# Optimization experiments

Hardware: AMD Instinct MI355X
Metric: run time of the kernel (lower is better)

## Reference

```python
import jax, jax.numpy as jnp
import numpy as np

N = 20000      # nodes
E = 200000     # edges (before self loops)
H = 8          # heads
C = 256        # out_channels per head
IN = 256       # in_channels
OUT = 250      # final linear out


def setup_inputs() -> dict:
    key = jax.random.key(0)
    ks = jax.random.split(key, 8)
    x = jax.random.normal(ks[0], (N, IN), jnp.float32)
    edge_index = jax.random.randint(ks[1], (2, E), 0, N)
    # GATConv params (lin has no bias in PyG; bias is on the conv output)
    W_gat = jax.random.normal(ks[2], (IN, H * C), jnp.float32) * 0.02
    att_src = jax.random.normal(ks[3], (H, C), jnp.float32) * 0.1
    att_dst = jax.random.normal(ks[4], (H, C), jnp.float32) * 0.1
    b_gat = jnp.zeros((H * C,), jnp.float32)
    # conv1: 1x1 conv with 1 in/out channel -> scalar weight + scalar bias
    conv_w = jax.random.normal(ks[5], (), jnp.float32)
    conv_b = jnp.zeros((), jnp.float32)
    W_lin = jax.random.normal(ks[6], (C, OUT), jnp.float32) * 0.02
    b_lin = jnp.zeros((OUT,), jnp.float32)
    return dict(x=x, edge_index=edge_index, W_gat=W_gat, att_src=att_src,
                att_dst=att_dst, b_gat=b_gat, conv_w=conv_w, conv_b=conv_b,
                W_lin=W_lin, b_lin=b_lin)


def reference(x, edge_index, W_gat, att_src, att_dst, b_gat, conv_w, conv_b, W_lin, b_lin):
    # --- GATConv (PyG defaults: add_self_loops=True, negative_slope=0.2, concat=True) ---
    loops = jnp.arange(N)
    src = jnp.concatenate([edge_index[0], loops])  # [E+N]
    dst = jnp.concatenate([edge_index[1], loops])
    xh = (x @ W_gat).reshape(N, H, C)              # [N,H,C]
    a_s = jnp.einsum('nhc,hc->nh', xh, att_src)    # [N,H]
    a_d = jnp.einsum('nhc,hc->nh', xh, att_dst)
    e = jax.nn.leaky_relu(a_s[src] + a_d[dst], 0.2)  # [E+N, H]
    # segment softmax over edges sharing a destination node
    m = jax.ops.segment_max(e, dst, num_segments=N)
    m = jnp.where(jnp.isfinite(m), m, 0.0)
    ex = jnp.exp(e - m[dst])
    s = jax.ops.segment_sum(ex, dst, num_segments=N)
    alpha = ex / (s[dst] + 1e-16)                  # [E+N, H]
    msg = xh[src] * alpha[:, :, None]              # [E+N, H, C]  (dominant traffic)
    agg = jax.ops.segment_sum(msg, dst, num_segments=N)  # [N,H,C]
    agg = agg + b_gat.reshape(H, C)
    # --- head split / pool / 1x1 conv / head softmax / fuse ---
    z = agg.transpose(1, 0, 2)                     # [H,N,C]  (torch z is [H,1,N,C])
    pooled = z.mean(axis=(1, 2))                   # [H] global avg pool
    g = jax.nn.relu(pooled * conv_w + conv_b)
    w = jax.nn.softmax(g, axis=0)                  # softmax over heads (dim=0)
    fuse = jnp.einsum('hnc,h->nc', z, w)           # sum over heads of z * w
    Hf = jax.nn.relu(fuse + x)                     # residual with input features
    return Hf @ W_lin + b_lin                      # [N, 250]
```

## Files before the change

### kernel.cpp

```cpp
#include <hip/hip_runtime.h>
#include <hip/hip_bf16.h>


typedef __attribute__((ext_vector_type(8))) short short8v;
typedef __attribute__((ext_vector_type(4))) float float4v;

__device__ __forceinline__ unsigned f2bfu(float f) {
  unsigned u = __float_as_uint(f);
  return (u + 0x7fffu + ((u >> 16) & 1u)) >> 16;
}
__device__ __forceinline__ float bfu_lo(unsigned u) { return __uint_as_float(u << 16); }
__device__ __forceinline__ float bfu_hi(unsigned u) { return __uint_as_float(u & 0xffff0000u); }
__device__ __forceinline__ unsigned pack2(float a, float b) { return f2bfu(a) | (f2bfu(b) << 16); }

__device__ __forceinline__ void ld8(const float* p, float* v) {
  float4 a = ((const float4*)p)[0], b = ((const float4*)p)[1];
  v[0] = a.x; v[1] = a.y; v[2] = a.z; v[3] = a.w;
  v[4] = b.x; v[5] = b.y; v[6] = b.z; v[7] = b.w;
}

__device__ __forceinline__ float bcast(float x, int e) {
  return __uint_as_float((unsigned)__builtin_amdgcn_readlane((int)__float_as_uint(x), e));
}

__device__ __forceinline__ void gll16(const void* g, void* l) {
  __builtin_amdgcn_global_load_lds(
      (__attribute__((address_space(1))) void*)const_cast<void*>(g),
      (__attribute__((address_space(3))) void*)(l), 16, 0, 0);
}

__global__ __launch_bounds__(256) void prep1_kernel(
    const float* __restrict__ W_lin, short* __restrict__ wlT,
    const float* __restrict__ W, const float* __restrict__ att_s,
    const float* __restrict__ att_d, float* __restrict__ ws_s,
    float* __restrict__ ws_d, float* __restrict__ ws_r,
    const int* __restrict__ ei, int* __restrict__ deg) {
  __shared__ float smem[4096];
  int b = blockIdx.x;
  int t = threadIdx.x;
  if (b < 64) {
    float (*tile)[33] = (float(*)[33])smem;
    int tx = t & 31, ty = t >> 5;
    int c0 = (b & 7) * 32, r0 = (b >> 3) * 32;
    #pragma unroll
    for (int j = ty; j < 32; j += 8) {
      int r = r0 + j, c = c0 + tx;
      tile[j][tx] = (c < 250) ? W_lin[(size_t)r * 250 + c] : 0.f;
    }
    __syncthreads();
    #pragma unroll
    for (int j = ty; j < 32; j += 8) {
      int c = c0 + j, r = r0 + tx;
      wlT[(size_t)c * 256 + r] = (short)f2bfu(tile[tx][j]);
    }
  } else if (b < 96) {
    float* sas = smem;
    float* sad = smem + 2048;
    for (int i = t; i < 2048; i += 256) { sas[i] = att_s[i]; sad[i] = att_d[i]; }
    __syncthreads();
    int kk = t >> 5, h = (t >> 2) & 7, q = t & 3;
    int k = (b - 64) * 8 + kk;
    const float4* wr = (const float4*)(W + (size_t)k * 2048 + h * 256 + q * 64);
    const float* as = sas + h * 256 + q * 64;
    const float* ad = sad + h * 256 + q * 64;
    float s = 0.f, dd = 0.f, r = 0.f;
    #pragma unroll
    for (int c4 = 0; c4 < 16; ++c4) {
      float4 wv = wr[c4];
      int c = c4 * 4;
      s  += wv.x * as[c] + wv.y * as[c + 1] + wv.z * as[c + 2] + wv.w * as[c + 3];
      dd += wv.x * ad[c] + wv.y * ad[c + 1] + wv.z * ad[c + 2] + wv.w * ad[c + 3];
      r  += wv.x + wv.y + wv.z + wv.w;
    }
    #pragma unroll
    for (int off = 1; off < 4; off <<= 1) {
      s += __shfl_xor(s, off);
      dd += __shfl_xor(dd, off);
      r += __shfl_xor(r, off);
    }
    if (q == 0) {
      int g = k * 8 + h;
      ws_s[g] = s;
      ws_d[g] = dd;
      ws_r[g] = r;
    }
  } else {
    int e = (b - 96) * 256 + t;
    if (e < 200000) atomicAdd(&deg[ei[200000 + e]], 1);
  }
}

__global__ __launch_bounds__(256) void asd_kernel(const float* __restrict__ x,
    const float* __restrict__ ws_s, const float* __restrict__ ws_d,
    const float* __restrict__ ws_r, float* __restrict__ a_s,
    float* __restrict__ a_d, float* __restrict__ rs, short* __restrict__ x_bf) {
  __shared__ float ls[2048], ld2[2048], lr[2048];
  int tid = threadIdx.x;
  for (int i = tid; i < 2048; i += 256) { ls[i] = ws_s[i]; ld2[i] = ws_d[i]; lr[i] = ws_r[i]; }
  __syncthreads();
  int node = blockIdx.x * 32 + (tid >> 3);
  int h = tid & 7;
  const float4* xr = (const float4*)(x + (size_t)node * 256);
  float as = 0.f, ad = 0.f, rr = 0.f;
  #pragma unroll 1
  for (int g = 0; g < 8; ++g) {
    bool own = (g == h);
    int bufi[16];
    #pragma unroll
    for (int j = 0; j < 8; ++j) {
      int k4 = g * 8 + j;
      float4 v = xr[k4];
      int k8 = k4 * 32 + h;
      as += v.x * ls[k8] + v.y * ls[k8 + 8] + v.z * ls[k8 + 16] + v.w * ls[k8 + 24];
      ad += v.x * ld2[k8] + v.y * ld2[k8 + 8] + v.z * ld2[k8 + 16] + v.w * ld2[k8 + 24];
      rr += v.x * lr[k8] + v.y * lr[k8 + 8] + v.z * lr[k8 + 16] + v.w * lr[k8 + 24];
      bufi[2 * j] = (int)pack2(v.x, v.y);
      bufi[2 * j + 1] = (int)pack2(v.z, v.w);
    }
    if (own) {
      int4* dst = (int4*)(x_bf + (size_t)node * 256 + h * 32);
      dst[0] = make_int4(bufi[0], bufi[1], bufi[2], bufi[3]);
      dst[1] = make_int4(bufi[4], bufi[5], bufi[6], bufi[7]);
      dst[2] = make_int4(bufi[8], bufi[9], bufi[10], bufi[11]);
      dst[3] = make_int4(bufi[12], bufi[13], bufi[14], bufi[15]);
    }
  }
  a_s[node * 8 + h] = as;
  a_d[node * 8 + h] = ad;
  rs[node * 8 + h] = rr;
}

__global__ __launch_bounds__(256, 2) void gemm_fused_kernel(
    const short* __restrict__ u, const short* __restrict__ wmixT,
    const short* __restrict__ wlT, short* __restrict__ Hf,
    float* __restrict__ out, const float* __restrict__ fb,
    const float* __restrict__ x, const float* __restrict__ b_lin, int M) {
  __shared__ short lA[64 * 128];
  __shared__ short lB[256 * 128];
  int tid = threadIdx.x;
  int wave = tid >> 6, lane = tid & 63;
  int m0 = blockIdx.x << 6;
  int lr = lane & 15, lq = lane >> 4;
  int lrow4 = lane >> 4;
  int pch = lane & 15;

  float4v acc[4][4];
  #pragma unroll
  for (int i = 0; i < 4; ++i)
    #pragma unroll
    for (int j = 0; j < 4; ++j) acc[i][j] = (float4v){0.f, 0.f, 0.f, 0.f};

  int rowlA[4], growA[4], logA[4];
  #pragma unroll
  for (int it = 0; it < 4; ++it) {
    rowlA[it] = wave * 16 + it * 4 + lrow4;
    int grow = m0 + rowlA[it];
    if (grow >= M) grow = M - 1;
    growA[it] = grow;
    logA[it] = pch ^ (rowlA[it] & 7);
  }
  int rowB[16], logB[16];
  #pragma unroll
  for (int it = 0; it < 16; ++it) {
    rowB[it] = wave * 64 + it * 4 + lrow4;
    logB[it] = pch ^ (rowB[it] & 7);
  }

  for (int t = 0; t < 16; ++t) {
    int k0 = t << 7;
    __syncthreads();
    #pragma unroll
    for (int it = 0; it < 4; ++it)
      gll16(u + (size_t)growA[it] * 2048 + logA[it] * 8 + k0, lA + (wave * 16 + it * 4) * 128);
    #pragma unroll
    for (int it = 0; it < 16; ++it)
      gll16(wmixT + (size_t)rowB[it] * 2048 + logB[it] * 8 + k0, lB + (wave * 64 + it * 4) * 128);
    __syncthreads();
    #pragma unroll
    for (int ks = 0; ks < 4; ++ks) {
      int phys = ((ks * 4 + lq) ^ (lr & 7)) * 8;
      short8v af[4], bfv[4];
      #pragma unroll
      for (int i = 0; i < 4; ++i)
        af[i] = *(const short8v*)(lA + (i * 16 + lr) * 128 + phys);
      #pragma unroll
      for (int j = 0; j < 4; ++j)
        bfv[j] = *(const short8v*)(lB + (wave * 64 + j * 16 + lr) * 128 + phys);
      #pragma unroll
      for (int i = 0; i < 4; ++i)
        #pragma unroll
        for (int j = 0; j < 4; ++j)
          acc[i][j] = __builtin_amdgcn_mfma_f32_16x16x32_bf16(af[i], bfv[j], acc[i][j], 0, 0, 0);
    }
  }
  #pragma unroll
  for (int i = 0; i < 4; ++i) {
    #pragma unroll
    for (int jj = 0; jj < 4; ++jj) {
      int row = m0 + i * 16 + lq * 4 + jj;
      if (row >= M) continue;
      #pragma unroll
      for (int j = 0; j < 4; ++j) {
        int col = wave * 64 + j * 16 + lr;
        float o = acc[i][j][jj] + fb[col] + x[(size_t)row * 256 + col];
        Hf[(size_t)row * 256 + col] = (short)f2bfu(fmaxf(o, 0.f));
      }
    }
  }

  #pragma unroll
  for (int i = 0; i < 4; ++i)
    #pragma unroll
    for (int j = 0; j < 4; ++j) acc[i][j] = (float4v){0.f, 0.f, 0.f, 0.f};

  for (int t = 0; t < 2; ++t) {
    int k0 = t << 7;
    __syncthreads();
    #pragma unroll
    for (int it = 0; it < 4; ++it)
      gll16(Hf + (size_t)growA[it] * 256 + logA[it] * 8 + k0, lA + (wave * 16 + it * 4) * 128);
    #pragma unroll
    for (int it = 0; it < 16; ++it)
      gll16(wlT + (size_t)rowB[it] * 256 + logB[it] * 8 + k0, lB + (wave * 64 + it * 4) * 128);
    __syncthreads();
    #pragma unroll
    for (int ks = 0; ks < 4; ++ks) {
      int phys = ((ks * 4 + lq) ^ (lr & 7)) * 8;
      short8v af[4], bfv[4];
      #pragma unroll
      for (int i = 0; i < 4; ++i)
        af[i] = *(const short8v*)(lA + (i * 16 + lr) * 128 + phys);
      #pragma unroll
      for (int j = 0; j < 4; ++j)
        bfv[j] = *(const short8v*)(lB + (wave * 64 + j * 16 + lr) * 128 + phys);
      #pragma unroll
      for (int i = 0; i < 4; ++i)
        #pragma unroll
        for (int j = 0; j < 4; ++j)
          acc[i][j] = __builtin_amdgcn_mfma_f32_16x16x32_bf16(af[i], bfv[j], acc[i][j], 0, 0, 0);
    }
  }
  #pragma unroll
  for (int i = 0; i < 4; ++i) {
    #pragma unroll
    for (int jj = 0; jj < 4; ++jj) {
      int row = m0 + i * 16 + lq * 4 + jj;
      if (row >= M) continue;
      #pragma unroll
      for (int j = 0; j < 4; ++j) {
        int col = wave * 64 + j * 16 + lr;
        if (col < 250) out[(size_t)row * 250 + col] = acc[i][j][jj] + b_lin[col];
      }
    }
  }
}


__global__ __launch_bounds__(1024) void scan_kernel(const int* __restrict__ deg,
                                                    int* __restrict__ rowptr,
                                                    int* __restrict__ cursor, int n) {
  __shared__ int part[1024];
  int t = threadIdx.x;
  int base = t * 20;
  int loc[20];
  int run = 0;
  #pragma unroll
  for (int j = 0; j < 20; ++j) {
    int idx = base + j;
    int v = (idx < n) ? deg[idx] : 0;
    loc[j] = run;
    run += v;
  }
  part[t] = run;
  __syncthreads();
  for (int off = 1; off < 1024; off <<= 1) {
    int add = (t >= off) ? part[t - off] : 0;
    __syncthreads();
    part[t] += add;
    __syncthreads();
  }
  int off0 = (t > 0) ? part[t - 1] : 0;
  #pragma unroll
  for (int j = 0; j < 20; ++j) {
    int idx = base + j;
    if (idx < n) {
      int v = off0 + loc[j];
      rowptr[idx] = v;
      cursor[idx] = v;
    }
  }
  if (t == 1023) rowptr[n] = part[1023];
}

__global__ void scatter_kernel(const int* __restrict__ ei, int* __restrict__ cursor,
                               int* __restrict__ csr_src, int E) {
  int e = blockIdx.x * 256 + threadIdx.x;
  if (e < E) {
    int pos = atomicAdd(&cursor[ei[E + e]], 1);
    csr_src[pos] = ei[e];
  }
}

__global__ __launch_bounds__(256) void alphaz_kernel(
    const short* __restrict__ x_bf, const float* __restrict__ a_s,
    const float* __restrict__ a_d, const float* __restrict__ rs,
    const int* __restrict__ rowptr, const int* __restrict__ csr,
    short* __restrict__ u, float* __restrict__ pp) {
  int d = blockIdx.x * 4 + (threadIdx.x >> 6);
  int lane = threadIdx.x & 63;
  int half = lane >> 5;
  int cl = (lane & 31) * 8;
  int beg = rowptr[d];
  int deg = rowptr[d + 1] - beg;
  int nb = deg + 1;

  float ad8[8];
  ld8(a_d + (size_t)d * 8, ad8);

  float acc[8][8];
  #pragma unroll
  for (int h = 0; h < 8; ++h)
    #pragma unroll
    for (int c = 0; c < 8; ++c) acc[h][c] = 0.f;
  float s8[8] = {0, 0, 0, 0, 0, 0, 0, 0};
  float p8[8] = {0, 0, 0, 0, 0, 0, 0, 0};

  for (int base = 0; base < nb; base += 64) {
    int i = base + lane;
    bool act = i < nb;
    int srcv = d;
    if (i < deg) srcv = csr[beg + i];
    float ex[8];
    {
      float t8[8], r8[8];
      ld8(a_s + (size_t)srcv * 8, t8);
      ld8(rs + (size_t)srcv * 8, r8);
      #pragma unroll
      for (int h = 0; h < 8; ++h) {
        float e = t8[h] + ad8[h];
        e = (e > 0.f) ? e : 0.2f * e;
        float xx = act ? __expf(e) : 0.f;
        ex[h] = xx;
        s8[h] += xx;
        p8[h] += xx * r8[h];
      }
    }
    int cnt = nb - base;
    if (cnt > 64) cnt = 64;
    int e = 0;
    for (; e + 1 < cnt; e += 2) {
      int s0 = __builtin_amdgcn_readlane(srcv, e);
      int s1 = __builtin_amdgcn_readlane(srcv, e + 1);
      int ss = half ? s1 : s0;
      uint4 v = *(const uint4*)(x_bf + (size_t)ss * 256 + cl);
      float q[8];
      #pragma unroll
      for (int h = 0; h < 8; ++h) {
        float qa = bcast(ex[h], e), qb = bcast(ex[h], e + 1);
        q[h] = half ? qb : qa;
      }
      float xv[8];
      xv[0] = bfu_lo(v.x); xv[1] = bfu_hi(v.x);
      xv[2] = bfu_lo(v.y); xv[3] = bfu_hi(v.y);
      xv[4] = bfu_lo(v.z); xv[5] = bfu_hi(v.z);
      xv[6] = bfu_lo(v.w); xv[7] = bfu_hi(v.w);
      #pragma unroll
      for (int h = 0; h < 8; ++h)
        #pragma unroll
        for (int c = 0; c < 8; ++c) acc[h][c] += q[h] * xv[c];
    }
    if (e < cnt) {
      int s0 = __builtin_amdgcn_readlane(srcv, e);
      uint4 v = *(const uint4*)(x_bf + (size_t)s0 * 256 + cl);
      float q[8];
      #pragma unroll
      for (int h = 0; h < 8; ++h) q[h] = half ? 0.f : bcast(ex[h], e);
      float xv[8];
      xv[0] = bfu_lo(v.x); xv[1] = bfu_hi(v.x);
      xv[2] = bfu_lo(v.y); xv[3] = bfu_hi(v.y);
      xv[4] = bfu_lo(v.z); xv[5] = bfu_hi(v.z);
      xv[6] = bfu_lo(v.w); xv[7] = bfu_hi(v.w);
      #pragma unroll
      for (int h = 0; h < 8; ++h)
        #pragma unroll
        for (int c = 0; c < 8; ++c) acc[h][c] += q[h] * xv[c];
    }
  }

  #pragma unroll
  for (int h = 0; h < 8; ++h)
    #pragma unroll
    for (int c = 0; c < 8; ++c) acc[h][c] += __shfl_xor(acc[h][c], 32);
  #pragma unroll
  for (int off = 1; off < 64; off <<= 1)
    #pragma unroll
    for (int h = 0; h < 8; ++h) {
      s8[h] += __shfl_xor(s8[h], off);
      p8[h] += __shfl_xor(p8[h], off);
    }
  float inv[8];
  #pragma unroll
  for (int h = 0; h < 8; ++h) inv[h] = 1.f / (s8[h] + 1e-16f);

  if (half == 0) {
    #pragma unroll
    for (int h = 0; h < 8; ++h) {
      uint4 ov;
      ov.x = pack2(acc[h][0] * inv[h], acc[h][1] * inv[h]);
      ov.y = pack2(acc[h][2] * inv[h], acc[h][3] * inv[h]);
      ov.z = pack2(acc[h][4] * inv[h], acc[h][5] * inv[h]);
      ov.w = pack2(acc[h][6] * inv[h], acc[h][7] * inv[h]);
      *(uint4*)(u + (size_t)d * 2048 + h * 256 + cl) = ov;
    }
  }
  if (lane == 0) {
    float pn[8];
    #pragma unroll
    for (int h = 0; h < 8; ++h) pn[h] = p8[h] * inv[h];
    ((float4*)(pp + (size_t)d * 8))[0] = make_float4(pn[0], pn[1], pn[2], pn[3]);
    ((float4*)(pp + (size_t)d * 8))[1] = make_float4(pn[4], pn[5], pn[6], pn[7]);
  }
}

__global__ __launch_bounds__(256) void reduce_pp_kernel(const float* __restrict__ pp,
                                                        float* __restrict__ pooled) {
  int tid = threadIdx.x;
  float loc[8] = {0, 0, 0, 0, 0, 0, 0, 0};
  for (int r = blockIdx.x * 256 + tid; r < 20000; r += 80 * 256) {
    float t[8];
    ld8(pp + (size_t)r * 8, t);
    #pragma unroll
    for (int h = 0; h < 8; ++h) loc[h] += t[h];
  }
  #pragma unroll
  for (int off = 1; off < 64; off <<= 1)
    #pragma unroll
    for (int h = 0; h < 8; ++h) loc[h] += __shfl_xor(loc[h], off);
  __shared__ float sred[4][8];
  int wave = tid >> 6, lane = tid & 63;
  if (lane == 0) {
    #pragma unroll
    for (int h = 0; h < 8; ++h) sred[wave][h] = loc[h];
  }
  __syncthreads();
  if (tid < 8) {
    atomicAdd(&pooled[tid], sred[0][tid] + sred[1][tid] + sred[2][tid] + sred[3][tid]);
  }
}

__global__ __launch_bounds__(256) void headwfb_kernel(const float* __restrict__ pooled,
    const float* __restrict__ b_gat, const float* __restrict__ conv_w,
    const float* __restrict__ conv_b, float* __restrict__ wsoft,
    float* __restrict__ fb) {
  __shared__ float sb[8];
  __shared__ float sw[8];
  int t = threadIdx.x;
  float v = 0.f;
  #pragma unroll
  for (int j = 0; j < 8; ++j) v += b_gat[t * 8 + j];
  #pragma unroll
  for (int off = 1; off < 32; off <<= 1) v += __shfl_xor(v, off);
  if ((t & 31) == 0) sb[t >> 5] = v;
  __syncthreads();
  if (t == 0) {
    const float invNC = 1.0f / (20000.0f * 256.0f);
    float g[8];
    float mx = -1e30f;
    #pragma unroll
    for (int h = 0; h < 8; ++h) {
      float pm = (pooled[h] + 20000.0f * sb[h]) * invNC;
      float gv = pm * conv_w[0] + conv_b[0];
      gv = fmaxf(gv, 0.f);
      g[h] = gv;
      mx = fmaxf(mx, gv);
    }
    float ssum = 0.f;
    #pragma unroll
    for (int h = 0; h < 8; ++h) { g[h] = __expf(g[h] - mx); ssum += g[h]; }
    #pragma unroll
    for (int h = 0; h < 8; ++h) {
      float w = g[h] / ssum;
      wsoft[h] = w;
      sw[h] = w;
    }
  }
  __syncthreads();
  float a = 0.f;
  #pragma unroll
  for (int h = 0; h < 8; ++h) a += sw[h] * b_gat[h * 256 + t];
  fb[t] = a;
}

__global__ void wmix_kernel(const float* __restrict__ W, const float* __restrict__ wsoft,
                            short* __restrict__ out) {
  __shared__ float tile[32][33];
  int tx = threadIdx.x, ty = threadIdx.y;
  int h = blockIdx.z;
  float wh = wsoft[h];
  int c0 = blockIdx.x * 32, k0 = blockIdx.y * 32;
  #pragma unroll
  for (int j = ty; j < 32; j += 8)
    tile[j][tx] = W[(size_t)(k0 + j) * 2048 + h * 256 + c0 + tx];
  __syncthreads();
  #pragma unroll
  for (int j = ty; j < 32; j += 8)
    out[(size_t)(c0 + j) * 2048 + h * 256 + k0 + tx] = (short)f2bfu(wh * tile[tx][j]);
}

extern "C" void kernel_launch(void* const* d_in, const int* in_sizes, int n_in,
                              void* d_out, int out_size, void* d_ws, size_t ws_size,
                              hipStream_t stream) {
  (void)in_sizes; (void)n_in; (void)out_size; (void)ws_size;
  const float* x      = (const float*)d_in[0];
  const int*   ei     = (const int*)d_in[1];
  const float* W_gat  = (const float*)d_in[2];
  const float* att_s  = (const float*)d_in[3];
  const float* att_d  = (const float*)d_in[4];
  const float* b_gat  = (const float*)d_in[5];
  const float* conv_w = (const float*)d_in[6];
  const float* conv_b = (const float*)d_in[7];
  const float* W_lin  = (const float*)d_in[8];
  const float* b_lin  = (const float*)d_in[9];
  float* out = (float*)d_out;

  char* p = (char*)d_ws;
  size_t off = 0;
  auto alloc = [&](size_t bytes) -> void* {
    void* r = p + off;
    off = (off + bytes + 255) & ~(size_t)255;
    return r;
  };
  short* x_bf   = (short*)alloc((size_t)20000 * 256 * 2);
  short* wmixT  = (short*)alloc((size_t)256 * 2048 * 2);
  short* wlT    = (short*)alloc((size_t)256 * 256 * 2);
  float* ws_s   = (float*)alloc(2048 * 4);
  float* ws_d   = (float*)alloc(2048 * 4);
  float* ws_r   = (float*)alloc(2048 * 4);
  float* a_s    = (float*)alloc((size_t)20000 * 8 * 4);
  float* a_d    = (float*)alloc((size_t)20000 * 8 * 4);
  float* rs     = (float*)alloc((size_t)20000 * 8 * 4);
  int*   deg    = (int*)alloc(20000 * 4);
  float* pooled = (float*)alloc(8 * 4);
  float* wsoft  = (float*)alloc(8 * 4);
  float* fb     = (float*)alloc(256 * 4);
  int*   rowptr = (int*)alloc(20001 * 4);
  int*   cursor = (int*)alloc(20000 * 4);
  int*   csr    = (int*)alloc(200000 * 4);
  float* pp     = (float*)alloc((size_t)20000 * 8 * 4);
  short* u      = (short*)alloc((size_t)20000 * 2048 * 2);
  short* Hf     = x_bf;

  hipMemsetAsync(deg, 0, 20000 * 4, stream);
  hipMemsetAsync(pooled, 0, 8 * 4, stream);

  prep1_kernel<<<878, 256, 0, stream>>>(W_lin, wlT, W_gat, att_s, att_d,
                                        ws_s, ws_d, ws_r, ei, deg);
  scan_kernel<<<1, 1024, 0, stream>>>(deg, rowptr, cursor, 20000);
  asd_kernel<<<625, 256, 0, stream>>>(x, ws_s, ws_d, ws_r, a_s, a_d, rs, x_bf);
  scatter_kernel<<<782, 256, 0, stream>>>(ei, cursor, csr, 200000);
  alphaz_kernel<<<5000, 256, 0, stream>>>(x_bf, a_s, a_d, rs, rowptr, csr, u, pp);
  reduce_pp_kernel<<<80, 256, 0, stream>>>(pp, pooled);
  headwfb_kernel<<<1, 256, 0, stream>>>(pooled, b_gat, conv_w, conv_b, wsoft, fb);
  wmix_kernel<<<dim3(8, 8, 8), dim3(32, 8), 0, stream>>>(W_gat, wsoft, wmixT);
  gemm_fused_kernel<<<313, 256, 0, stream>>>(u, wmixT, wlT, Hf, out, fb, x, b_lin, 20000);
}
```

Measured before the change: 208.2 us.

## Compute pooled projection from aggregated features instead of per-node rs term

Drops the per-node rs dot product from the asd kernel and its gather in alphaz. The pooled contribution is now computed after aggregation by dotting the normalized aggregate against ws_r with a wave reduction. Alphaz is also restructured so each lane owns 4 channels and processes one edge per iteration, replacing the two-edges-per-iteration half-wave split and its final cross-half shuffle. This lowers register pressure and removes one memory stream, but issues narrower loads and adds a per-node reduction.

After: 194.4 us. -6.6%, faster.

```diff
diff --git a/kernel.cpp b/kernel.cpp
--- a/kernel.cpp
+++ b/kernel.cpp
@@ -92,16 +92,15 @@
 
 __global__ __launch_bounds__(256) void asd_kernel(const float* __restrict__ x,
     const float* __restrict__ ws_s, const float* __restrict__ ws_d,
-    const float* __restrict__ ws_r, float* __restrict__ a_s,
-    float* __restrict__ a_d, float* __restrict__ rs, short* __restrict__ x_bf) {
-  __shared__ float ls[2048], ld2[2048], lr[2048];
+    float* __restrict__ a_s, float* __restrict__ a_d, short* __restrict__ x_bf) {
+  __shared__ float ls[2048], ld2[2048];
   int tid = threadIdx.x;
-  for (int i = tid; i < 2048; i += 256) { ls[i] = ws_s[i]; ld2[i] = ws_d[i]; lr[i] = ws_r[i]; }
+  for (int i = tid; i < 2048; i += 256) { ls[i] = ws_s[i]; ld2[i] = ws_d[i]; }
   __syncthreads();
   int node = blockIdx.x * 32 + (tid >> 3);
   int h = tid & 7;
   const float4* xr = (const float4*)(x + (size_t)node * 256);
-  float as = 0.f, ad = 0.f, rr = 0.f;
+  float as = 0.f, ad = 0.f;
   #pragma unroll 1
   for (int g = 0; g < 8; ++g) {
     bool own = (g == h);
@@ -113,7 +112,6 @@
       int k8 = k4 * 32 + h;
       as += v.x * ls[k8] + v.y * ls[k8 + 8] + v.z * ls[k8 + 16] + v.w * ls[k8 + 24];
       ad += v.x * ld2[k8] + v.y * ld2[k8 + 8] + v.z * ld2[k8 + 16] + v.w * ld2[k8 + 24];
-      rr += v.x * lr[k8] + v.y * lr[k8 + 8] + v.z * lr[k8 + 16] + v.w * lr[k8 + 24];
       bufi[2 * j] = (int)pack2(v.x, v.y);
       bufi[2 * j + 1] = (int)pack2(v.z, v.w);
     }
@@ -127,7 +125,6 @@
   }
   a_s[node * 8 + h] = as;
   a_d[node * 8 + h] = ad;
-  rs[node * 8 + h] = rr;
 }
 
 __global__ __launch_bounds__(256, 2) void gemm_fused_kernel(
@@ -303,13 +300,12 @@
 
 __global__ __launch_bounds__(256) void alphaz_kernel(
     const short* __restrict__ x_bf, const float* __restrict__ a_s,
-    const float* __restrict__ a_d, const float* __restrict__ rs,
+    const float* __restrict__ a_d, const float* __restrict__ ws_r,
     const int* __restrict__ rowptr, const int* __restrict__ csr,
     short* __restrict__ u, float* __restrict__ pp) {
   int d = blockIdx.x * 4 + (threadIdx.x >> 6);
   int lane = threadIdx.x & 63;
-  int half = lane >> 5;
-  int cl = (lane & 31) * 8;
+  int cl = lane * 4;
   int beg = rowptr[d];
   int deg = rowptr[d + 1] - beg;
   int nb = deg + 1;
@@ -317,13 +313,12 @@
   float ad8[8];
   ld8(a_d + (size_t)d * 8, ad8);
 
-  float acc[8][8];
+  float acc[8][4];
   #pragma unroll
   for (int h = 0; h < 8; ++h)
     #pragma unroll
-    for (int c = 0; c < 8; ++c) acc[h][c] = 0.f;
+    for (int c = 0; c < 4; ++c) acc[h][c] = 0.f;
   float s8[8] = {0, 0, 0, 0, 0, 0, 0, 0};
-  float p8[8] = {0, 0, 0, 0, 0, 0, 0, 0};
 
   for (int base = 0; base < nb; base += 64) {
     int i = base + lane;
@@ -332,9 +327,8 @@
     if (i < deg) srcv = csr[beg + i];
     float ex[8];
     {
-      float t8[8], r8[8];
+      float t8[8];
       ld8(a_s + (size_t)srcv * 8, t8);
-      ld8(rs + (size_t)srcv * 8, r8);
       #pragma unroll
       for (int h = 0; h < 8; ++h) {
         float e = t8[h] + ad8[h];
@@ -342,83 +336,66 @@
         float xx = act ? __expf(e) : 0.f;
         ex[h] = xx;
         s8[h] += xx;
-        p8[h] += xx * r8[h];
       }
     }
     int cnt = nb - base;
     if (cnt > 64) cnt = 64;
-    int e = 0;
-    for (; e + 1 < cnt; e += 2) {
-      int s0 = __builtin_amdgcn_readlane(srcv, e);
-      int s1 = __builtin_amdgcn_readlane(srcv, e + 1);
-      int ss = half ? s1 : s0;
-      uint4 v = *(const uint4*)(x_bf + (size_t)ss * 256 + cl);
+    for (int e = 0; e < cnt; ++e) {
+      int sb = __builtin_amdgcn_readlane(srcv, e);
+      uint2 v = *(const uint2*)(x_bf + (size_t)sb * 256 + cl);
       float q[8];
       #pragma unroll
+      for (int h = 0; h < 8; ++h) q[h] = bcast(ex[h], e);
+      float xv0 = bfu_lo(v.x), xv1 = bfu_hi(v.x);
+      float xv2 = bfu_lo(v.y), xv3 = bfu_hi(v.y);
+      #pragma unroll
       for (int h = 0; h < 8; ++h) {
-        float qa = bcast(ex[h], e), qb = bcast(ex[h], e + 1);
-        q[h] = half ? qb : qa;
+        acc[h][0] += q[h] * xv0;
+        acc[h][1] += q[h] * xv1;
+        acc[h][2] += q[h] * xv2;
+        acc[h][3] += q[h] * xv3;
       }
-      float xv[8];
-      xv[0] = bfu_lo(v.x); xv[1] = bfu_hi(v.x);
-      xv[2] = bfu_lo(v.y); xv[3] = bfu_hi(v.y);
-      xv[4] = bfu_lo(v.z); xv[5] = bfu_hi(v.z);
-      xv[6] = bfu_lo(v.w); xv[7] = bfu_hi(v.w);
-      #pragma unroll
-      for (int h = 0; h < 8; ++h)
-        #pragma unroll
-        for (int c = 0; c < 8; ++c) acc[h][c] += q[h] * xv[c];
-    }
-    if (e < cnt) {
-      int s0 = __builtin_amdgcn_readlane(srcv, e);
-      uint4 v = *(const uint4*)(x_bf + (size_t)s0 * 256 + cl);
-      float q[8];
-      #pragma unroll
-      for (int h = 0; h < 8; ++h) q[h] = half ? 0.f : bcast(ex[h], e);
-      float xv[8];
-      xv[0] = bfu_lo(v.x); xv[1] = bfu_hi(v.x);
-      xv[2] = bfu_lo(v.y); xv[3] = bfu_hi(v.y);
-      xv[4] = bfu_lo(v.z); xv[5] = bfu_hi(v.z);
-      xv[6] = bfu_lo(v.w); xv[7] = bfu_hi(v.w);
-      #pragma unroll
-      for (int h = 0; h < 8; ++h)
-        #pragma unroll
-        for (int c = 0; c < 8; ++c) acc[h][c] += q[h] * xv[c];
-    }
-  }
-
-  #pragma unroll
-  for (int h = 0; h < 8; ++h)
-    #pragma unroll
-    for (int c = 0; c < 8; ++c) acc[h][c] += __shfl_xor(acc[h][c], 32);
+    }
+  }
+
   #pragma unroll
   for (int off = 1; off < 64; off <<= 1)
     #pragma unroll
-    for (int h = 0; h < 8; ++h) {
-      s8[h] += __shfl_xor(s8[h], off);
-      p8[h] += __shfl_xor(p8[h], off);
-    }
+    for (int h = 0; h < 8; ++h) s8[h] += __shfl_xor(s8[h], off);
   float inv[8];
   #pragma unroll
   for (int h = 0; h < 8; ++h) inv[h] = 1.f / (s8[h] + 1e-16f);
 
-  if (half == 0) {
-    #pragma unroll
-    for (int h = 0; h < 8; ++h) {
-      uint4 ov;
-      ov.x = pack2(acc[h][0] * inv[h], acc[h][1] * inv[h]);
-      ov.y = pack2(acc[h][2] * inv[h], acc[h][3] * inv[h]);
-      ov.z = pack2(acc[h][4] * inv[h], acc[h][5] * inv[h]);
-      ov.w = pack2(acc[h][6] * inv[h], acc[h][7] * inv[h]);
-      *(uint4*)(u + (size_t)d * 2048 + h * 256 + cl) = ov;
-    }
-  }
+  #pragma unroll
+  for (int h = 0; h < 8; ++h) {
+    uint2 ov;
+    ov.x = pack2(acc[h][0] * inv[h], acc[h][1] * inv[h]);
+    ov.y = pack2(acc[h][2] * inv[h], acc[h][3] * inv[h]);
+    *(uint2*)(u + (size_t)d * 2048 + h * 256 + cl) = ov;
+  }
+
+  float ppl[8] = {0, 0, 0, 0, 0, 0, 0, 0};
+  {
+    const float4* wr = (const float4*)(ws_r + (size_t)cl * 8);
+    #pragma unroll
+    for (int c = 0; c < 4; ++c) {
+      float4 wa = wr[c * 2], wb = wr[c * 2 + 1];
+      float zc[8];
+      #pragma unroll
+      for (int h = 0; h < 8; ++h) zc[h] = acc[h][c] * inv[h];
+      ppl[0] += zc[0] * wa.x; ppl[1] += zc[1] * wa.y;
+      ppl[2] += zc[2] * wa.z; ppl[3] += zc[3] * wa.w;
+      ppl[4] += zc[4] * wb.x; ppl[5] += zc[5] * wb.y;
+      ppl[6] += zc[6] * wb.z; ppl[7] += zc[7] * wb.w;
+    }
+  }
+  #pragma unroll
+  for (int off = 1; off < 64; off <<= 1)
+    #pragma unroll
+    for (int h = 0; h < 8; ++h) ppl[h] += __shfl_xor(ppl[h], off);
   if (lane == 0) {
-    float pn[8];
-    #pragma unroll
-    for (int h = 0; h < 8; ++h) pn[h] = p8[h] * inv[h];
-    ((float4*)(pp + (size_t)d * 8))[0] = make_float4(pn[0], pn[1], pn[2], pn[3]);
-    ((float4*)(pp + (size_t)d * 8))[1] = make_float4(pn[4], pn[5], pn[6], pn[7]);
+    ((float4*)(pp + (size_t)d * 8))[0] = make_float4(ppl[0], ppl[1], ppl[2], ppl[3]);
+    ((float4*)(pp + (size_t)d * 8))[1] = make_float4(ppl[4], ppl[5], ppl[6], ppl[7]);
   }
 }
 
@@ -538,7 +515,6 @@
   float* ws_r   = (float*)alloc(2048 * 4);
   float* a_s    = (float*)alloc((size_t)20000 * 8 * 4);
   float* a_d    = (float*)alloc((size_t)20000 * 8 * 4);
-  float* rs     = (float*)alloc((size_t)20000 * 8 * 4);
   int*   deg    = (int*)alloc(20000 * 4);
   float* pooled = (float*)alloc(8 * 4);
   float* wsoft  = (float*)alloc(8 * 4);
@@ -556,9 +532,9 @@
   prep1_kernel<<<878, 256, 0, stream>>>(W_lin, wlT, W_gat, att_s, att_d,
                                         ws_s, ws_d, ws_r, ei, deg);
   scan_kernel<<<1, 1024, 0, stream>>>(deg, rowptr, cursor, 20000);
-  asd_kernel<<<625, 256, 0, stream>>>(x, ws_s, ws_d, ws_r, a_s, a_d, rs, x_bf);
+  asd_kernel<<<625, 256, 0, stream>>>(x, ws_s, ws_d, a_s, a_d, x_bf);
   scatter_kernel<<<782, 256, 0, stream>>>(ei, cursor, csr, 200000);
-  alphaz_kernel<<<5000, 256, 0, stream>>>(x_bf, a_s, a_d, rs, rowptr, csr, u, pp);
+  alphaz_kernel<<<5000, 256, 0, stream>>>(x_bf, a_s, a_d, ws_r, rowptr, csr, u, pp);
   reduce_pp_kernel<<<80, 256, 0, stream>>>(pp, pooled);
   headwfb_kernel<<<1, 256, 0, stream>>>(pooled, b_gat, conv_w, conv_b, wsoft, fb);
   wmix_kernel<<<dim3(8, 8, 8), dim3(32, 8), 0, stream>>>(W_gat, wsoft, wmixT);
```
